# Optimization experiments

Measured on AMD Instinct MI355X. Metric: run time of the kernel, lower is better.

## Reference

```python
import jax, jax.numpy as jnp
import numpy as np

L = 5          # num GNN layers
N = 50000      # nodes
E = 400000     # edges
D = 128        # emb_dim == in_dim
H = 2 * D      # GIN MLP hidden
BOND_DIMS = [5, 6, 2]          # OGB bond feature vocab sizes
OFFSETS = jnp.array([0, 5, 11])  # offsets into concatenated bond table (size 13)
BN_EPS = 1e-5


def batchnorm(h, gamma, beta):
    # training-mode BatchNorm1d: biased batch statistics over node axis
    mu = h.mean(axis=0)
    var = h.var(axis=0)
    return gamma * (h - mu) * jax.lax.rsqrt(var + BN_EPS) + beta


def setup_inputs() -> dict:
    key = jax.random.key(0)
    ks = jax.random.split(key, 8)
    s = 0.05
    return {
        "x": jax.random.normal(ks[0], (N, D), jnp.float32),
        "edge_index": jax.random.randint(ks[1], (2, E), 0, N),
        "edge_attr": jax.random.randint(ks[2], (E, 3), 0, 2),
        # stacked per-layer params (all layers have in_dim == emb_dim == D)
        "W1": jax.random.normal(ks[3], (L, D, H), jnp.float32) * s,
        "b1": jnp.zeros((L, H), jnp.float32),
        "g1": jnp.ones((L, H), jnp.float32),   # BN inside MLP
        "bb1": jnp.zeros((L, H), jnp.float32),
        "W2": jax.random.normal(ks[4], (L, H, D), jnp.float32) * s,
        "b2": jnp.zeros((L, D), jnp.float32),
        "eps": jnp.zeros((L,), jnp.float32),    # GIN eps (init 0)
        "bond_emb": jax.random.normal(ks[5], (L, sum(BOND_DIMS), D), jnp.float32) * s,
        "g2": jnp.ones((L, D), jnp.float32),    # outer per-layer BN
        "bb2": jnp.zeros((L, D), jnp.float32),
    }


def reference(x, edge_index, edge_attr, W1, b1, g1, bb1, W2, b2, eps, bond_emb, g2, bb2):
    src, dst = edge_index[0], edge_index[1]
    e_idx = edge_attr + OFFSETS[None, :]  # [E,3] indices into concat bond table

    def gin_layer(h, l):
        # BondEncoder: sum of 3 categorical embeddings -> [E,D]
        edge_emb = bond_emb[l][e_idx].sum(axis=1)
        # message: relu(x_j + edge_attr), aggregated (add) at destination
        msg = jax.nn.relu(h[src] + edge_emb)
        agg = jax.ops.segment_sum(msg, dst, num_segments=N)
        z = (1.0 + eps[l]) * h + agg
        # GIN MLP: Linear -> BN -> ReLU -> Linear
        z = jax.nn.relu(batchnorm(z @ W1[l] + b1[l], g1[l], bb1[l]))
        z = z @ W2[l] + b2[l]
        # outer per-layer BN
        return batchnorm(z, g2[l], bb2[l])

    h = x
    for l in range(L - 1):
        h = jax.nn.relu(gin_layer(h, l))  # relu between layers
    h = gin_layer(h, L - 1)               # no relu on last layer for 'gin'
    return h  # JK='last'
```

## Files before the change

### kernel.cpp

```cpp
#include <hip/hip_runtime.h>
#include <hip/hip_bf16.h>

#define NNODES 50000
#define MPAD 50048
#define NEDGES 400000
#define DIM 128
#define HID 256
#define NLAYERS 5
#define BONDSZ 13
#define NCOMBO 60
#define BN_EPS 1e-5f
#define NCHUNK 49
#define INVN (1.0f / 50000.0f)

typedef __bf16 bf16x8 __attribute__((ext_vector_type(8)));
typedef __bf16 bf16x4v __attribute__((ext_vector_type(4)));
typedef float f32x4 __attribute__((ext_vector_type(4)));

#define GLOAD16(dst, addr) \
    asm volatile("global_load_dwordx4 %0, %1, off" : "=v"(dst) : "v"(addr) : "memory")

template<int N> __device__ __forceinline__ void vmwaitN() {
    if constexpr (N == 16)      asm volatile("s_waitcnt vmcnt(16)" ::: "memory");
    else if constexpr (N == 32) asm volatile("s_waitcnt vmcnt(32)" ::: "memory");
    else static_assert(N == 16 || N == 32, "unsupported vmcnt");
    __builtin_amdgcn_sched_barrier(0);
}

__global__ __launch_bounds__(256) void hist_kernel(
    const int* __restrict__ dst, int* __restrict__ deg)
{
    int e = blockIdx.x * 256 + threadIdx.x;
    if (e < NEDGES) atomicAdd(&deg[dst[e]], 1);
}

__global__ __launch_bounds__(256) void scan_sum(
    const int* __restrict__ deg, int* __restrict__ partial)
{
    __shared__ int red[256];
    int base = blockIdx.x * 1024;
    int s = 0;
    for (int i = threadIdx.x; i < 1024; i += 256) {
        int idx = base + i;
        if (idx < NNODES) s += deg[idx];
    }
    red[threadIdx.x] = s;
    __syncthreads();
    for (int off = 128; off > 0; off >>= 1) {
        if (threadIdx.x < off) red[threadIdx.x] += red[threadIdx.x + off];
        __syncthreads();
    }
    if (threadIdx.x == 0) partial[blockIdx.x] = red[0];
}

__global__ void scan_part(int* __restrict__ partial, int n, int* __restrict__ rowptr_last)
{
    if (threadIdx.x == 0) {
        int acc = 0;
        for (int i = 0; i < n; i++) { int v = partial[i]; partial[i] = acc; acc += v; }
        rowptr_last[0] = acc;
    }
}

__global__ __launch_bounds__(256) void scan_write(
    const int* __restrict__ deg, const int* __restrict__ partial,
    int* __restrict__ row_ptr)
{
    __shared__ int red[256];
    int base = blockIdx.x * 1024;
    int t = threadIdx.x;
    int v[4];
    int s = 0;
    #pragma unroll
    for (int j = 0; j < 4; j++) {
        int idx = base + t * 4 + j;
        v[j] = (idx < NNODES) ? deg[idx] : 0;
        s += v[j];
    }
    red[t] = s;
    __syncthreads();
    for (int off = 1; off < 256; off <<= 1) {
        int x = (t >= off) ? red[t - off] : 0;
        __syncthreads();
        red[t] += x;
        __syncthreads();
    }
    int ex = red[t] - s + partial[blockIdx.x];
    #pragma unroll
    for (int j = 0; j < 4; j++) {
        int idx = base + t * 4 + j;
        if (idx < NNODES) row_ptr[idx] = ex;
        ex += v[j];
    }
}

__global__ __launch_bounds__(256) void scatter_kernel(
    const int* __restrict__ src, const int* __restrict__ dst,
    const int* __restrict__ eattr, const int* __restrict__ row_ptr,
    int* __restrict__ cursor, int2* __restrict__ epack)
{
    int e = blockIdx.x * 256 + threadIdx.x;
    if (e >= NEDGES) return;
    int d = dst[e];
    int pos = row_ptr[d] + atomicAdd(&cursor[d], 1);
    int a0 = eattr[e * 3 + 0];
    int a1 = eattr[e * 3 + 1];
    int a2 = eattr[e * 3 + 2];
    epack[pos] = make_int2(src[e], a0 * 12 + a1 * 2 + a2);
}

__global__ __launch_bounds__(256) void wsplit_kernel(
    const float* __restrict__ W1, const float* __restrict__ W2,
    __bf16* __restrict__ bt1h, __bf16* __restrict__ bt1l,
    __bf16* __restrict__ bt2h, __bf16* __restrict__ bt2l)
{
    int gid = blockIdx.x * 256 + threadIdx.x;
    const int total1 = NLAYERS * DIM * HID;
    if (gid < total1) {
        int n = gid % HID; int k = (gid / HID) % DIM; int l = gid / (DIM * HID);
        float w = W1[gid];
        __bf16 hi = (__bf16)w;
        int o = (l * HID + n) * DIM + k;
        bt1h[o] = hi; bt1l[o] = (__bf16)(w - (float)hi);
    } else {
        int g = gid - total1;
        if (g < NLAYERS * HID * DIM) {
            int n = g % DIM; int k = (g / DIM) % HID; int l = g / (HID * DIM);
            float w = W2[g];
            __bf16 hi = (__bf16)w;
            int o = (l * DIM + n) * HID + k;
            bt2h[o] = hi; bt2l[o] = (__bf16)(w - (float)hi);
        }
    }
}

template<int TRANS>
__global__ __launch_bounds__(1024) void agg_combine(
    const float* __restrict__ hin,
    const __bf16* __restrict__ hb,
    const int* __restrict__ row_ptr, const int2* __restrict__ epack,
    const float* __restrict__ bond,
    const float* __restrict__ epsv, int lidx,
    const float* __restrict__ csIn, const float* __restrict__ cqIn,
    const float* __restrict__ gamma, const float* __restrict__ beta,
    __bf16* __restrict__ zH, __bf16* __restrict__ zL,
    float* __restrict__ statsZero)
{
    __shared__ float T[BONDSZ * DIM];
    __shared__ float TC[NCOMBO * DIM];
    __shared__ float scs[DIM], shs[DIM];

    for (int i = threadIdx.x; i < BONDSZ * DIM; i += 1024) T[i] = bond[i];
    if (TRANS && threadIdx.x < DIM) {
        int c = threadIdx.x;
        float mu = csIn[c] * INVN;
        float var = cqIn[c] * INVN - mu * mu;
        float sv = gamma[c] * rsqrtf(var + BN_EPS);
        scs[c] = sv; shs[c] = beta[c] - mu * sv;
    }
    if (blockIdx.x == 0 && threadIdx.x < 768) statsZero[threadIdx.x] = 0.f;
    __syncthreads();
    for (int i = threadIdx.x; i < NCOMBO * DIM; i += 1024) {
        int cb = i >> 7, c = i & 127;
        int a0 = cb / 12, r = cb - a0 * 12;
        TC[i] = T[a0 * DIM + c] + T[(5 + (r >> 1)) * DIM + c] + T[(11 + (r & 1)) * DIM + c];
    }
    __syncthreads();

    const int wv = threadIdx.x >> 6;
    const int half = (threadIdx.x >> 5) & 1;
    const int li = threadIdx.x & 31;
    const int node = blockIdx.x * 32 + wv * 2 + half;
    if (node >= NNODES) return;
    const int f = li * 4;

    float4 sc4 = make_float4(1.f, 1.f, 1.f, 1.f);
    float4 sh4 = make_float4(0.f, 0.f, 0.f, 0.f);
    if (TRANS) { sc4 = *(const float4*)&scs[f]; sh4 = *(const float4*)&shs[f]; }

    float ax = 0.f, ay = 0.f, az = 0.f, aw = 0.f;
    const int s = row_ptr[node];
    const int e2 = row_ptr[node + 1];
    int i = s;
    for (; i + 3 < e2; i += 4) {
        int2 ev[4];
        ev[0] = epack[i];     ev[1] = epack[i + 1];
        ev[2] = epack[i + 2]; ev[3] = epack[i + 3];
        float4 gv[4], tv[4];
        #pragma unroll
        for (int u = 0; u < 4; u++) {
            if (TRANS) {
                bf16x4v gb = *(const bf16x4v*)&hb[(size_t)ev[u].x * DIM + f];
                gv[u] = make_float4((float)gb[0], (float)gb[1], (float)gb[2], (float)gb[3]);
            } else {
                gv[u] = *(const float4*)&hin[(size_t)ev[u].x * DIM + f];
            }
            tv[u] = *(const float4*)&TC[ev[u].y * DIM + f];
        }
        #pragma unroll
        for (int u = 0; u < 4; u++) {
            float4 g = gv[u], t = tv[u];
            if (TRANS) {
                g.x = fmaxf(g.x * sc4.x + sh4.x, 0.f); g.y = fmaxf(g.y * sc4.y + sh4.y, 0.f);
                g.z = fmaxf(g.z * sc4.z + sh4.z, 0.f); g.w = fmaxf(g.w * sc4.w + sh4.w, 0.f);
            }
            ax += fmaxf(g.x + t.x, 0.f);
            ay += fmaxf(g.y + t.y, 0.f);
            az += fmaxf(g.z + t.z, 0.f);
            aw += fmaxf(g.w + t.w, 0.f);
        }
    }
    for (; i < e2; i++) {
        int2 ev = epack[i];
        float4 g;
        if (TRANS) {
            bf16x4v gb = *(const bf16x4v*)&hb[(size_t)ev.x * DIM + f];
            g = make_float4((float)gb[0], (float)gb[1], (float)gb[2], (float)gb[3]);
        } else {
            g = *(const float4*)&hin[(size_t)ev.x * DIM + f];
        }
        float4 t = *(const float4*)&TC[ev.y * DIM + f];
        if (TRANS) {
            g.x = fmaxf(g.x * sc4.x + sh4.x, 0.f); g.y = fmaxf(g.y * sc4.y + sh4.y, 0.f);
            g.z = fmaxf(g.z * sc4.z + sh4.z, 0.f); g.w = fmaxf(g.w * sc4.w + sh4.w, 0.f);
        }
        ax += fmaxf(g.x + t.x, 0.f);
        ay += fmaxf(g.y + t.y, 0.f);
        az += fmaxf(g.z + t.z, 0.f);
        aw += fmaxf(g.w + t.w, 0.f);
    }
    float4 hv;
    if (TRANS) {
        bf16x4v hbv = *(const bf16x4v*)&hb[(size_t)node * DIM + f];
        hv = make_float4((float)hbv[0], (float)hbv[1], (float)hbv[2], (float)hbv[3]);
        hv.x = fmaxf(hv.x * sc4.x + sh4.x, 0.f); hv.y = fmaxf(hv.y * sc4.y + sh4.y, 0.f);
        hv.z = fmaxf(hv.z * sc4.z + sh4.z, 0.f); hv.w = fmaxf(hv.w * sc4.w + sh4.w, 0.f);
    } else {
        hv = *(const float4*)&hin[(size_t)node * DIM + f];
    }
    float ep = 1.0f + epsv[lidx];
    float z0 = ep * hv.x + ax, z1 = ep * hv.y + ay;
    float z2 = ep * hv.z + az, z3 = ep * hv.w + aw;
    __bf16 h0 = (__bf16)z0, h1 = (__bf16)z1, h2 = (__bf16)z2, h3 = (__bf16)z3;
    size_t o = (size_t)node * DIM + f;
    bf16x4v vh = {h0, h1, h2, h3};
    bf16x4v vl = {(__bf16)(z0 - (float)h0), (__bf16)(z1 - (float)h1),
                  (__bf16)(z2 - (float)h2), (__bf16)(z3 - (float)h3)};
    *(bf16x4v*)(zH + o) = vh;
    *(bf16x4v*)(zL + o) = vl;
}

template<int K, int NCOLS, int COLS, int TRANSFORM, int XB, int MINW, int WRITEF>
__global__ __launch_bounds__(256, MINW) void gemm_ps(
    const __bf16* __restrict__ AH, const __bf16* __restrict__ AL,
    const __bf16* __restrict__ AB,
    const __bf16* __restrict__ BTH, const __bf16* __restrict__ BTL,
    const float* __restrict__ bias,
    const float* __restrict__ csIn, const float* __restrict__ cqIn,
    const float* __restrict__ gamma, const float* __restrict__ beta,
    float* __restrict__ outF, __bf16* __restrict__ outB,
    float* __restrict__ colsum, float* __restrict__ colsumsq)
{
    constexpr int KC  = K / 8;
    constexpr int NK  = K / 32;
    constexpr int NJ  = COLS / 16;
    constexpr int NYB = MPAD / 64;
    constexpr int WS  = NJ * 4 * (WRITEF ? 2 : 1);

    __shared__ __bf16 sBH[COLS * K], sBL[COLS * K];
    __shared__ float scs[TRANSFORM ? K : 1], shs[TRANSFORM ? K : 1];

    const int bid  = blockIdx.x;
    const int xcd  = bid & 7;
    const int grp  = bid >> 3;
    const int xb   = grp % XB;
    const int pb   = (grp / XB) * 8 + xcd;
    const int tid  = threadIdx.x;
    const int lane = tid & 63;
    const int wv   = tid >> 6;
    const int rowL = lane & 15;
    const int quad = lane >> 4;
    const int n0   = xb * COLS;

    bf16x8 pH[2][TRANSFORM ? 1 : NK], pL[2][TRANSFORM ? 1 : NK];
    bf16x8 pB[2][TRANSFORM ? NK : 1];

#define A_ISSUE(tt) do {                                                      \
    const size_t rb_ = ((size_t)(pb + 256 * (tt)) * 64 + wv * 16 + rowL) * K  \
                       + quad * 8;                                            \
    _Pragma("unroll")                                                         \
    for (int ks = 0; ks < NK; ks++) {                                         \
        if constexpr (!TRANSFORM) {                                           \
            GLOAD16(pH[(tt) & 1][ks], AH + rb_ + ks * 32);                    \
            GLOAD16(pL[(tt) & 1][ks], AL + rb_ + ks * 32);                    \
        } else {                                                              \
            GLOAD16(pB[(tt) & 1][ks], AB + rb_ + ks * 32);                    \
        }                                                                     \
    }                                                                         \
} while (0)

    A_ISSUE(0);

    float bb[NJ];
    #pragma unroll
    for (int j = 0; j < NJ; j++) bb[j] = bias[n0 + j * 16 + rowL];
    if (TRANSFORM) {
        for (int c = tid; c < K; c += 256) {
            float mu = csIn[c] * INVN;
            float var = cqIn[c] * INVN - mu * mu;
            float sv = gamma[c] * rsqrtf(var + BN_EPS);
            scs[c] = sv; shs[c] = beta[c] - mu * sv;
        }
    }

    #pragma unroll
    for (int it = 0; it < (COLS * KC) / 256; it++) {
        int c = it * 256 + tid;
        int col = c / KC, kq = c % KC;
        int slot = col * KC + (kq ^ (col & (KC - 1)));
        size_t g = (size_t)(n0 + col) * K + kq * 8;
        *(bf16x8*)(sBH + slot * 8) = *(const bf16x8*)(BTH + g);
        *(bf16x8*)(sBL + slot * 8) = *(const bf16x8*)(BTL + g);
    }
    __syncthreads();
    __builtin_amdgcn_sched_barrier(0);

    float stS[NJ] = {}, stQ[NJ] = {};

#define STRIPE(tt) do {                                                       \
    if (pb + 256 * (tt) < NYB) {                                              \
        if constexpr ((tt) > 0) { vmwaitN<WS>(); }                            \
        if constexpr ((tt) < 3) {                                             \
            if (pb + 256 * ((tt) + 1) < NYB) A_ISSUE((tt) + 1);               \
        }                                                                     \
        f32x4 acc[NJ] = {};                                                   \
        _Pragma("unroll")                                                     \
        for (int ks = 0; ks < NK; ks++) {                                     \
            bf16x8 aH8, aL8;                                                  \
            if constexpr (!TRANSFORM) {                                       \
                aH8 = pH[(tt) & 1][ks];                                       \
                aL8 = pL[(tt) & 1][ks];                                       \
            } else {                                                          \
                const int kb = ks * 32 + quad * 8;                            \
                float4 s0 = *(const float4*)&scs[kb];                         \
                float4 s1 = *(const float4*)&scs[kb + 4];                     \
                float4 t0 = *(const float4*)&shs[kb];                         \
                float4 t1 = *(const float4*)&shs[kb + 4];                     \
                float sv[8] = {s0.x, s0.y, s0.z, s0.w, s1.x, s1.y, s1.z, s1.w}; \
                float tv[8] = {t0.x, t0.y, t0.z, t0.w, t1.x, t1.y, t1.z, t1.w}; \
                _Pragma("unroll")                                             \
                for (int e = 0; e < 8; e++) {                                 \
                    float v = fmaxf((float)pB[(tt) & 1][ks][e] * sv[e] + tv[e], 0.f); \
                    __bf16 hi = (__bf16)v;                                    \
                    aH8[e] = hi;                                              \
                    aL8[e] = (__bf16)(v - (float)hi);                         \
                }                                                             \
            }                                                                 \
            const int kqr = ks * 4 + quad;                                    \
            _Pragma("unroll")                                                 \
            for (int j = 0; j < NJ; j++) {                                    \
                int col = j * 16 + rowL;                                      \
                int slot = col * KC + (kqr ^ (col & (KC - 1)));               \
                bf16x8 bH = *(const bf16x8*)(sBH + slot * 8);                 \
                bf16x8 bL = *(const bf16x8*)(sBL + slot * 8);                 \
                acc[j] = __builtin_amdgcn_mfma_f32_16x16x32_bf16(aH8, bH, acc[j], 0, 0, 0); \
                acc[j] = __builtin_amdgcn_mfma_f32_16x16x32_bf16(aL8, bH, acc[j], 0, 0, 0); \
                acc[j] = __builtin_amdgcn_mfma_f32_16x16x32_bf16(aH8, bL, acc[j], 0, 0, 0); \
            }                                                                 \
        }                                                                     \
           \
               \
        const int r0t = (pb + 256 * (tt)) * 64 + wv * 16 + quad * 4;          \
        _Pragma("unroll")                                                     \
        for (int j = 0; j < NJ; j++) {                                        \
            const int colL = j * 16 + rowL;                                   \
            _Pragma("unroll")                                                 \
            for (int r = 0; r < 4; r++) {                                     \
                const int rr = r0t + r;                                       \
                float v = acc[j][r] + bb[j];                                  \
                size_t oidx = (size_t)rr * NCOLS + n0 + colL;                 \
                if constexpr (WRITEF) outF[oidx] = v;                         \
                outB[oidx] = (__bf16)v;                                       \
                if (rr < NNODES) { stS[j] += v; stQ[j] += v * v; }            \
            }                                                                 \
        }                                                                     \
    }                                                                         \
} while (0)

    STRIPE(0);
    STRIPE(1);
    STRIPE(2);
    STRIPE(3);

#undef STRIPE
#undef A_ISSUE

    #pragma unroll
    for (int j = 0; j < NJ; j++) {
        stS[j] += __shfl_xor(stS[j], 16); stS[j] += __shfl_xor(stS[j], 32);
        stQ[j] += __shfl_xor(stQ[j], 16); stQ[j] += __shfl_xor(stQ[j], 32);
    }
    __syncthreads();
    float* red = (float*)sBH;
    if (quad == 0) {
        #pragma unroll
        for (int j = 0; j < NJ; j++) {
            const int colL = j * 16 + rowL;
            red[(wv * 2 + 0) * COLS + colL] = stS[j];
            red[(wv * 2 + 1) * COLS + colL] = stQ[j];
        }
    }
    __syncthreads();
    if (tid < COLS) {
        float s = red[0 * COLS + tid] + red[2 * COLS + tid] +
                  red[4 * COLS + tid] + red[6 * COLS + tid];
        float q = red[1 * COLS + tid] + red[3 * COLS + tid] +
                  red[5 * COLS + tid] + red[7 * COLS + tid];
        atomicAdd(&colsum[n0 + tid], s);
        atomicAdd(&colsumsq[n0 + tid], q);
    }
}

__global__ __launch_bounds__(256) void bn_out(
    const float* __restrict__ y2, const float* __restrict__ csIn,
    const float* __restrict__ cqIn, const float* __restrict__ gamma,
    const float* __restrict__ beta, float* __restrict__ out)
{
    __shared__ float scs[DIM], shs[DIM];
    if (threadIdx.x < DIM) {
        int c = threadIdx.x;
        float mu = csIn[c] * INVN;
        float var = cqIn[c] * INVN - mu * mu;
        float sv = gamma[c] * rsqrtf(var + BN_EPS);
        scs[c] = sv; shs[c] = beta[c] - mu * sv;
    }
    __syncthreads();
    int i = blockIdx.x * 256 + threadIdx.x;
    if (i >= NNODES * 32) return;
    int c = (i & 31) * 4;
    float4 v = *(const float4*)&y2[(size_t)i * 4];
    float4 s = *(const float4*)&scs[c];
    float4 t = *(const float4*)&shs[c];
    v.x = v.x * s.x + t.x;
    v.y = v.y * s.y + t.y;
    v.z = v.z * s.z + t.z;
    v.w = v.w * s.w + t.w;
    *(float4*)&out[(size_t)i * 4] = v;
}

extern "C" void kernel_launch(void* const* d_in, const int* in_sizes, int n_in,
                              void* d_out, int out_size, void* d_ws, size_t ws_size,
                              hipStream_t stream)
{
    const float* x    = (const float*)d_in[0];
    const int*   ei   = (const int*)d_in[1];
    const int*   ea   = (const int*)d_in[2];
    const float* W1   = (const float*)d_in[3];
    const float* b1   = (const float*)d_in[4];
    const float* g1   = (const float*)d_in[5];
    const float* bb1  = (const float*)d_in[6];
    const float* W2   = (const float*)d_in[7];
    const float* b2   = (const float*)d_in[8];
    const float* epsv = (const float*)d_in[9];
    const float* bond = (const float*)d_in[10];
    const float* g2   = (const float*)d_in[11];
    const float* bb2  = (const float*)d_in[12];
    float* out = (float*)d_out;

    const int* src = ei;
    const int* dstp = ei + NEDGES;

    float* ws = (float*)d_ws;
    float* y2    = ws;
    float* y1F   = y2 + (size_t)MPAD * DIM;
    float* stats = y1F + (size_t)MPAD * HID;
    __bf16* y1b  = (__bf16*)y1F;
    __bf16* zH   = (__bf16*)(stats + 2 * 768);
    __bf16* zL   = zH + (size_t)MPAD * DIM;
    __bf16* bt1h = zL + (size_t)MPAD * DIM;
    __bf16* bt1l = bt1h + (size_t)NLAYERS * DIM * HID;
    __bf16* bt2h = bt1l + (size_t)NLAYERS * DIM * HID;
    __bf16* bt2l = bt2h + (size_t)NLAYERS * HID * DIM;
    int* iws     = (int*)(bt2l + (size_t)NLAYERS * HID * DIM);
    int* deg     = iws;
    int* cursor  = deg + NNODES;
    int* row_ptr = cursor + NNODES;
    int* partial = row_ptr + NNODES + 1;
    int2* epack  = (int2*)(partial + 64);
    __bf16* y2b  = (__bf16*)(((uintptr_t)(epack + NEDGES) + 15) & ~(uintptr_t)15);

    hipMemsetAsync(deg, 0, 2 * NNODES * sizeof(int), stream);
    hist_kernel<<<(NEDGES + 255) / 256, 256, 0, stream>>>(dstp, deg);
    scan_sum<<<NCHUNK, 256, 0, stream>>>(deg, partial);
    scan_part<<<1, 64, 0, stream>>>(partial, NCHUNK, row_ptr + NNODES);
    scan_write<<<NCHUNK, 256, 0, stream>>>(deg, partial, row_ptr);
    scatter_kernel<<<(NEDGES + 255) / 256, 256, 0, stream>>>(
        src, dstp, ea, row_ptr, cursor, epack);
    wsplit_kernel<<<(2 * NLAYERS * DIM * HID + 255) / 256, 256, 0, stream>>>(
        W1, W2, bt1h, bt1l, bt2h, bt2l);

    for (int l = 0; l < NLAYERS; l++) {
        const int p = l & 1;
        float* cs1 = stats + p * 768;
        float* cq1 = cs1 + HID;
        float* cs2 = cq1 + HID;
        float* cq2 = cs2 + DIM;
        float* statsZ = stats + p * 768;

        if (l == 0) {
            agg_combine<0><<<(NNODES + 31) / 32, 1024, 0, stream>>>(
                x, nullptr, row_ptr, epack, bond + (size_t)l * BONDSZ * DIM,
                epsv, l, nullptr, nullptr, nullptr, nullptr, zH, zL, statsZ);
        } else {
            const int pp = (l - 1) & 1;
            float* pcs2 = stats + pp * 768 + 2 * HID;
            float* pcq2 = pcs2 + DIM;
            agg_combine<1><<<(NNODES + 31) / 32, 1024, 0, stream>>>(
                nullptr, y2b, row_ptr, epack, bond + (size_t)l * BONDSZ * DIM,
                epsv, l, pcs2, pcq2, g2 + (size_t)(l - 1) * DIM,
                bb2 + (size_t)(l - 1) * DIM, zH, zL, statsZ);
        }

        gemm_ps<DIM, HID, 64, 0, 4, 4, 0><<<1024, 256, 0, stream>>>(
            zH, zL, nullptr,
            bt1h + (size_t)l * HID * DIM, bt1l + (size_t)l * HID * DIM,
            b1 + (size_t)l * HID, nullptr, nullptr, nullptr, nullptr,
            nullptr, y1b, cs1, cq1);

        if (l < NLAYERS - 1) {
            gemm_ps<HID, DIM, 64, 1, 2, 2, 0><<<512, 256, 0, stream>>>(
                nullptr, nullptr, y1b,
                bt2h + (size_t)l * DIM * HID, bt2l + (size_t)l * DIM * HID,
                b2 + (size_t)l * DIM, cs1, cq1, g1 + (size_t)l * HID,
                bb1 + (size_t)l * HID, nullptr, y2b, cs2, cq2);
        } else {
            gemm_ps<HID, DIM, 64, 1, 2, 2, 1><<<512, 256, 0, stream>>>(
                nullptr, nullptr, y1b,
                bt2h + (size_t)l * DIM * HID, bt2l + (size_t)l * DIM * HID,
                b2 + (size_t)l * DIM, cs1, cq1, g1 + (size_t)l * HID,
                bb1 + (size_t)l * HID, y2, y2b, cs2, cq2);
        }
    }

    {
        float* cs2 = stats + 0 * 768 + 2 * HID;
        float* cq2 = cs2 + DIM;
        bn_out<<<(NNODES * 32 + 255) / 256, 256, 0, stream>>>(
            y2, cs2, cq2, g2 + (size_t)4 * DIM, bb2 + (size_t)4 * DIM, out);
    }
}
```

Measured before the change: 565.5 us.

## Pack edge records into one int, deepen GEMM2 prefetch, drop fp32 output

Edge records shrink from an int2 to a single int: the source index is shifted left by 6 and ORed with the bond combo index, which halves the per-edge index traffic in aggregation. The second GEMM gets a three-deep register prefetch pipeline for A tiles instead of two. The last layer no longer writes an fp32 copy of its output, and the final BN reads the bf16 copy instead. The bf16 final output loses precision, and the wider prefetch raises register pressure.

```diff
diff --git a/kernel.cpp b/kernel.cpp
--- a/kernel.cpp
+++ b/kernel.cpp
@@ -97,7 +97,7 @@
 __global__ __launch_bounds__(256) void scatter_kernel(
     const int* __restrict__ src, const int* __restrict__ dst,
     const int* __restrict__ eattr, const int* __restrict__ row_ptr,
-    int* __restrict__ cursor, int2* __restrict__ epack)
+    int* __restrict__ cursor, int* __restrict__ epack)
 {
     int e = blockIdx.x * 256 + threadIdx.x;
     if (e >= NEDGES) return;
@@ -106,7 +106,7 @@
     int a0 = eattr[e * 3 + 0];
     int a1 = eattr[e * 3 + 1];
     int a2 = eattr[e * 3 + 2];
-    epack[pos] = make_int2(src[e], a0 * 12 + a1 * 2 + a2);
+    epack[pos] = (src[e] << 6) | (a0 * 12 + a1 * 2 + a2);
 }
 
 __global__ __launch_bounds__(256) void wsplit_kernel(
@@ -138,7 +138,7 @@
 __global__ __launch_bounds__(1024) void agg_combine(
     const float* __restrict__ hin,
     const __bf16* __restrict__ hb,
-    const int* __restrict__ row_ptr, const int2* __restrict__ epack,
+    const int* __restrict__ row_ptr, const int* __restrict__ epack,
     const float* __restrict__ bond,
     const float* __restrict__ epsv, int lidx,
     const float* __restrict__ csIn, const float* __restrict__ cqIn,
@@ -183,19 +183,19 @@
     const int e2 = row_ptr[node + 1];
     int i = s;
     for (; i + 3 < e2; i += 4) {
-        int2 ev[4];
+        int ev[4];
         ev[0] = epack[i];     ev[1] = epack[i + 1];
         ev[2] = epack[i + 2]; ev[3] = epack[i + 3];
         float4 gv[4], tv[4];
         #pragma unroll
         for (int u = 0; u < 4; u++) {
             if (TRANS) {
-                bf16x4v gb = *(const bf16x4v*)&hb[(size_t)ev[u].x * DIM + f];
+                bf16x4v gb = *(const bf16x4v*)&hb[(size_t)(ev[u] >> 6) * DIM + f];
                 gv[u] = make_float4((float)gb[0], (float)gb[1], (float)gb[2], (float)gb[3]);
             } else {
-                gv[u] = *(const float4*)&hin[(size_t)ev[u].x * DIM + f];
+                gv[u] = *(const float4*)&hin[(size_t)(ev[u] >> 6) * DIM + f];
             }
-            tv[u] = *(const float4*)&TC[ev[u].y * DIM + f];
+            tv[u] = *(const float4*)&TC[(ev[u] & 63) * DIM + f];
         }
         #pragma unroll
         for (int u = 0; u < 4; u++) {
@@ -211,15 +211,15 @@
         }
     }
     for (; i < e2; i++) {
-        int2 ev = epack[i];
+        int ev = epack[i];
         float4 g;
         if (TRANS) {
-            bf16x4v gb = *(const bf16x4v*)&hb[(size_t)ev.x * DIM + f];
+            bf16x4v gb = *(const bf16x4v*)&hb[(size_t)(ev >> 6) * DIM + f];
             g = make_float4((float)gb[0], (float)gb[1], (float)gb[2], (float)gb[3]);
         } else {
-            g = *(const float4*)&hin[(size_t)ev.x * DIM + f];
-        }
-        float4 t = *(const float4*)&TC[ev.y * DIM + f];
+            g = *(const float4*)&hin[(size_t)(ev >> 6) * DIM + f];
+        }
+        float4 t = *(const float4*)&TC[(ev & 63) * DIM + f];
         if (TRANS) {
             g.x = fmaxf(g.x * sc4.x + sh4.x, 0.f); g.y = fmaxf(g.y * sc4.y + sh4.y, 0.f);
             g.z = fmaxf(g.z * sc4.z + sh4.z, 0.f); g.w = fmaxf(g.w * sc4.w + sh4.w, 0.f);
@@ -250,7 +250,7 @@
     *(bf16x4v*)(zL + o) = vl;
 }
 
-template<int K, int NCOLS, int COLS, int TRANSFORM, int XB, int MINW, int WRITEF>
+template<int K, int NCOLS, int COLS, int TRANSFORM, int XB, int MINW, int DEPTH>
 __global__ __launch_bounds__(256, MINW) void gemm_ps(
     const __bf16* __restrict__ AH, const __bf16* __restrict__ AL,
     const __bf16* __restrict__ AB,
@@ -258,14 +258,14 @@
     const float* __restrict__ bias,
     const float* __restrict__ csIn, const float* __restrict__ cqIn,
     const float* __restrict__ gamma, const float* __restrict__ beta,
-    float* __restrict__ outF, __bf16* __restrict__ outB,
+    __bf16* __restrict__ outB,
     float* __restrict__ colsum, float* __restrict__ colsumsq)
 {
     constexpr int KC  = K / 8;
     constexpr int NK  = K / 32;
     constexpr int NJ  = COLS / 16;
     constexpr int NYB = MPAD / 64;
-    constexpr int WS  = NJ * 4 * (WRITEF ? 2 : 1);
+    constexpr int WC  = (DEPTH == 3) ? 32 : 16;
 
     __shared__ __bf16 sBH[COLS * K], sBL[COLS * K];
     __shared__ float scs[TRANSFORM ? K : 1], shs[TRANSFORM ? K : 1];
@@ -282,8 +282,8 @@
     const int quad = lane >> 4;
     const int n0   = xb * COLS;
 
-    bf16x8 pH[2][TRANSFORM ? 1 : NK], pL[2][TRANSFORM ? 1 : NK];
-    bf16x8 pB[2][TRANSFORM ? NK : 1];
+    bf16x8 pH[DEPTH][TRANSFORM ? 1 : NK], pL[DEPTH][TRANSFORM ? 1 : NK];
+    bf16x8 pB[DEPTH][TRANSFORM ? NK : 1];
 
 #define A_ISSUE(tt) do {                                                      \
     const size_t rb_ = ((size_t)(pb + 256 * (tt)) * 64 + wv * 16 + rowL) * K  \
@@ -291,15 +291,18 @@
     _Pragma("unroll")                                                         \
     for (int ks = 0; ks < NK; ks++) {                                         \
         if constexpr (!TRANSFORM) {                                           \
-            GLOAD16(pH[(tt) & 1][ks], AH + rb_ + ks * 32);                    \
-            GLOAD16(pL[(tt) & 1][ks], AL + rb_ + ks * 32);                    \
+            GLOAD16(pH[(tt) % DEPTH][ks], AH + rb_ + ks * 32);                \
+            GLOAD16(pL[(tt) % DEPTH][ks], AL + rb_ + ks * 32);                \
         } else {                                                              \
-            GLOAD16(pB[(tt) & 1][ks], AB + rb_ + ks * 32);                    \
+            GLOAD16(pB[(tt) % DEPTH][ks], AB + rb_ + ks * 32);                \
         }                                                                     \
     }                                                                         \
 } while (0)
 
     A_ISSUE(0);
+    if constexpr (DEPTH == 3) {
+        if (pb + 256 < NYB) A_ISSUE(1);
+    }
 
     float bb[NJ];
     #pragma unroll
@@ -329,8 +332,11 @@
 
 #define STRIPE(tt) do {                                                       \
     if (pb + 256 * (tt) < NYB) {                                              \
-        if constexpr ((tt) > 0) { vmwaitN<WS>(); }                            \
-        if constexpr ((tt) < 3) {                                             \
+        if constexpr (DEPTH == 3 && (tt) + 2 <= 3) {                          \
+            if (pb + 256 * ((tt) + 2) < NYB) A_ISSUE((tt) + 2);               \
+        }                                                                     \
+        if constexpr ((tt) > 0) { vmwaitN<WC>(); }                            \
+        if constexpr (DEPTH == 2 && (tt) + 1 <= 3) {                          \
             if (pb + 256 * ((tt) + 1) < NYB) A_ISSUE((tt) + 1);               \
         }                                                                     \
         f32x4 acc[NJ] = {};                                                   \
@@ -338,8 +344,8 @@
         for (int ks = 0; ks < NK; ks++) {                                     \
             bf16x8 aH8, aL8;                                                  \
             if constexpr (!TRANSFORM) {                                       \
-                aH8 = pH[(tt) & 1][ks];                                       \
-                aL8 = pL[(tt) & 1][ks];                                       \
+                aH8 = pH[(tt) % DEPTH][ks];                                   \
+                aL8 = pL[(tt) % DEPTH][ks];                                   \
             } else {                                                          \
                 const int kb = ks * 32 + quad * 8;                            \
                 float4 s0 = *(const float4*)&scs[kb];                         \
@@ -350,7 +356,7 @@
                 float tv[8] = {t0.x, t0.y, t0.z, t0.w, t1.x, t1.y, t1.z, t1.w}; \
                 _Pragma("unroll")                                             \
                 for (int e = 0; e < 8; e++) {                                 \
-                    float v = fmaxf((float)pB[(tt) & 1][ks][e] * sv[e] + tv[e], 0.f); \
+                    float v = fmaxf((float)pB[(tt) % DEPTH][ks][e] * sv[e] + tv[e], 0.f); \
                     __bf16 hi = (__bf16)v;                                    \
                     aH8[e] = hi;                                              \
                     aL8[e] = (__bf16)(v - (float)hi);                         \
@@ -368,8 +374,7 @@
                 acc[j] = __builtin_amdgcn_mfma_f32_16x16x32_bf16(aH8, bL, acc[j], 0, 0, 0); \
             }                                                                 \
         }                                                                     \
-           \
-               \
+         \
         const int r0t = (pb + 256 * (tt)) * 64 + wv * 16 + quad * 4;          \
         _Pragma("unroll")                                                     \
         for (int j = 0; j < NJ; j++) {                                        \
@@ -378,9 +383,7 @@
             for (int r = 0; r < 4; r++) {                                     \
                 const int rr = r0t + r;                                       \
                 float v = acc[j][r] + bb[j];                                  \
-                size_t oidx = (size_t)rr * NCOLS + n0 + colL;                 \
-                if constexpr (WRITEF) outF[oidx] = v;                         \
-                outB[oidx] = (__bf16)v;                                       \
+                outB[(size_t)rr * NCOLS + n0 + colL] = (__bf16)v;             \
                 if (rr < NNODES) { stS[j] += v; stQ[j] += v * v; }            \
             }                                                                 \
         }                                                                     \
@@ -422,7 +425,7 @@
 }
 
 __global__ __launch_bounds__(256) void bn_out(
-    const float* __restrict__ y2, const float* __restrict__ csIn,
+    const __bf16* __restrict__ y2b, const float* __restrict__ csIn,
     const float* __restrict__ cqIn, const float* __restrict__ gamma,
     const float* __restrict__ beta, float* __restrict__ out)
 {
@@ -438,14 +441,15 @@
     int i = blockIdx.x * 256 + threadIdx.x;
     if (i >= NNODES * 32) return;
     int c = (i & 31) * 4;
-    float4 v = *(const float4*)&y2[(size_t)i * 4];
+    bf16x4v v4 = *(const bf16x4v*)&y2b[(size_t)i * 4];
     float4 s = *(const float4*)&scs[c];
     float4 t = *(const float4*)&shs[c];
-    v.x = v.x * s.x + t.x;
-    v.y = v.y * s.y + t.y;
-    v.z = v.z * s.z + t.z;
-    v.w = v.w * s.w + t.w;
-    *(float4*)&out[(size_t)i * 4] = v;
+    float4 o;
+    o.x = (float)v4[0] * s.x + t.x;
+    o.y = (float)v4[1] * s.y + t.y;
+    o.z = (float)v4[2] * s.z + t.z;
+    o.w = (float)v4[3] * s.w + t.w;
+    *(float4*)&out[(size_t)i * 4] = o;
 }
 
 extern "C" void kernel_launch(void* const* d_in, const int* in_sizes, int n_in,
@@ -471,8 +475,7 @@
     const int* dstp = ei + NEDGES;
 
     float* ws = (float*)d_ws;
-    float* y2    = ws;
-    float* y1F   = y2 + (size_t)MPAD * DIM;
+    float* y1F   = ws + (size_t)MPAD * DIM;
     float* stats = y1F + (size_t)MPAD * HID;
     __bf16* y1b  = (__bf16*)y1F;
     __bf16* zH   = (__bf16*)(stats + 2 * 768);
@@ -486,8 +489,8 @@
     int* cursor  = deg + NNODES;
     int* row_ptr = cursor + NNODES;
     int* partial = row_ptr + NNODES + 1;
-    int2* epack  = (int2*)(partial + 64);
-    __bf16* y2b  = (__bf16*)(((uintptr_t)(epack + NEDGES) + 15) & ~(uintptr_t)15);
+    int* epack   = partial + 64;
+    __bf16* y2b  = (__bf16*)(((uintptr_t)(epack + 2 * NEDGES) + 15) & ~(uintptr_t)15);
 
     hipMemsetAsync(deg, 0, 2 * NNODES * sizeof(int), stream);
     hist_kernel<<<(NEDGES + 255) / 256, 256, 0, stream>>>(dstp, deg);
@@ -521,31 +524,23 @@
                 bb2 + (size_t)(l - 1) * DIM, zH, zL, statsZ);
         }
 
-        gemm_ps<DIM, HID, 64, 0, 4, 4, 0><<<1024, 256, 0, stream>>>(
+        gemm_ps<DIM, HID, 64, 0, 4, 4, 2><<<1024, 256, 0, stream>>>(
             zH, zL, nullptr,
             bt1h + (size_t)l * HID * DIM, bt1l + (size_t)l * HID * DIM,
             b1 + (size_t)l * HID, nullptr, nullptr, nullptr, nullptr,
-            nullptr, y1b, cs1, cq1);
-
-        if (l < NLAYERS - 1) {
-            gemm_ps<HID, DIM, 64, 1, 2, 2, 0><<<512, 256, 0, stream>>>(
-                nullptr, nullptr, y1b,
-                bt2h + (size_t)l * DIM * HID, bt2l + (size_t)l * DIM * HID,
-                b2 + (size_t)l * DIM, cs1, cq1, g1 + (size_t)l * HID,
-                bb1 + (size_t)l * HID, nullptr, y2b, cs2, cq2);
-        } else {
-            gemm_ps<HID, DIM, 64, 1, 2, 2, 1><<<512, 256, 0, stream>>>(
-                nullptr, nullptr, y1b,
-                bt2h + (size_t)l * DIM * HID, bt2l + (size_t)l * DIM * HID,
-                b2 + (size_t)l * DIM, cs1, cq1, g1 + (size_t)l * HID,
-                bb1 + (size_t)l * HID, y2, y2b, cs2, cq2);
-        }
+            y1b, cs1, cq1);
+
+        gemm_ps<HID, DIM, 64, 1, 2, 2, 3><<<512, 256, 0, stream>>>(
+            nullptr, nullptr, y1b,
+            bt2h + (size_t)l * DIM * HID, bt2l + (size_t)l * DIM * HID,
+            b2 + (size_t)l * DIM, cs1, cq1, g1 + (size_t)l * HID,
+            bb1 + (size_t)l * HID, y2b, cs2, cq2);
     }
 
     {
         float* cs2 = stats + 0 * 768 + 2 * HID;
         float* cq2 = cs2 + DIM;
         bn_out<<<(NNODES * 32 + 255) / 256, 256, 0, stream>>>(
-            y2, cs2, cq2, g2 + (size_t)4 * DIM, bb2 + (size_t)4 * DIM, out);
-    }
-}
+            y2b, cs2, cq2, g2 + (size_t)4 * DIM, bb2 + (size_t)4 * DIM, out);
+    }
+}
```

Result: no change. 570.3 us (+0.9%).
